# Kernel tuning notes

Measured on AMD Instinct MI355X. Metric: run time of the kernel, lower is better.

Reference implementation:

```python
import jax, jax.numpy as jnp
import numpy as np

# Ternary quant: brevitas 2-bit narrow-range signed int quant with const scale 1.0
# -> q(x) = clamp(round(x), -1, 1), values in {-1, 0, 1}

def ternary(x):
    return jnp.clip(jnp.round(x), -1.0, 1.0)

def batchnorm(x, gamma, beta, eps=1e-5):
    # training-mode BatchNorm1d: batch statistics over dim 0 (biased var)
    mean = jnp.mean(x, axis=0)
    var = jnp.var(x, axis=0)
    return (x - mean) * jax.lax.rsqrt(var + eps) * gamma + beta

def tensornorm(x, w, b, eps=1e-4):
    # BNN-PYNQ TensorNorm: normalize over whole tensor (unbiased var), scalar affine
    mean = jnp.mean(x)
    var = jnp.var(x, ddof=1)
    return (x - mean) / jnp.sqrt(var + eps) * w + b


def setup_inputs() -> dict:
    key = jax.random.key(0)
    ks = jax.random.split(key, 4)
    B = 16384
    x = jax.random.uniform(ks[0], (B, 784), dtype=jnp.float32)          # MNIST-like in [0,1]
    W1 = 2.0 * jax.random.uniform(ks[1], (1024, 784), dtype=jnp.float32) - 1.0  # uniform(-1,1)
    W2 = 2.0 * jax.random.uniform(ks[2], (10, 1024), dtype=jnp.float32) - 1.0
    tnk1, tnk2 = jax.random.split(ks[3])
    return {
        "x": x,
        "W1": W1,
        "gamma1": jnp.ones((1024,), jnp.float32),
        "beta1": jnp.zeros((1024,), jnp.float32),
        "W2": W2,
        "gamma2": jnp.ones((10,), jnp.float32),
        "beta2": jnp.zeros((10,), jnp.float32),
        "tn_w": jax.random.uniform(tnk1, (1,), dtype=jnp.float32),
        "tn_b": jax.random.uniform(tnk2, (1,), dtype=jnp.float32),
    }


def reference(x, W1, gamma1, beta1, W2, gamma2, beta2, tn_w, tn_b):
    h = x.reshape(x.shape[0], -1)
    h = 2.0 * h - 1.0                 # input rescale to [-1,1]
    h = ternary(h)                    # QuantIdentity (2-bit act)
    h = h @ ternary(W1).T             # QuantLinear 784->1024, ternary weights, no bias
    h = batchnorm(h, gamma1, beta1)   # BatchNorm1d(1024)
    h = ternary(h)                    # QuantIdentity
    h = h @ ternary(W2).T             # QuantLinear 1024->10
    h = batchnorm(h, gamma2, beta2)   # BatchNorm1d(10)
    h = ternary(h)                    # QuantIdentity
    return tensornorm(h, tn_w, tn_b)  # TensorNorm
```

## Files before the change

### kernel.cpp

```cpp
#include <hip/hip_runtime.h>
#include <stdint.h>

typedef int i32x4 __attribute__((ext_vector_type(4)));
typedef short s16x8 __attribute__((ext_vector_type(8)));
typedef unsigned long long ull;

#define BB 16384
#define KD 784
#define KP 832
#define N1 1024
#define N2 10
#define NTOT (BB * N2)

#define OFF_AQ 0ULL
#define SZ_AQ (13631488ULL)
#define OFF_W1Q (OFF_AQ + SZ_AQ)
#define SZ_W1Q (851968ULL)
#define OFF_W2Q (OFF_W1Q + SZ_W1Q)
#define SZ_W2Q (16384ULL)
#define OFF_C1 (OFF_W2Q + SZ_W2Q)
#define SZ_C1 (33554432ULL)
#define OFF_STATS (OFF_C1 + SZ_C1)
#define SZ_STATS (16384ULL)
#define OFF_BN1 (OFF_STATS + SZ_STATS)
#define SZ_BN1 (16384ULL)
#define OFF_C2 (OFF_BN1 + SZ_BN1)
#define SZ_C2 (1048576ULL)
#define OFF_T2 (OFF_C2 + SZ_C2)
#define SZ_T2 (163840ULL)

__device__ __forceinline__ void async16(const void* g, void* l) {
  __builtin_amdgcn_global_load_lds((__attribute__((address_space(1))) void*)(void*)(g),
                                   (__attribute__((address_space(3))) void*)(l), 16, 0, 0);
}

__device__ __forceinline__ int8_t ternq(float v) {
  float q = rintf(v);
  return q > 0.5f ? 1 : (q < -0.5f ? -1 : 0);
}

__global__ void k0_quant(const float* __restrict__ x, const float* __restrict__ W1,
                         const float* __restrict__ W2, int8_t* __restrict__ Aq,
                         int8_t* __restrict__ W1q, int8_t* __restrict__ W2q,
                         int* __restrict__ stats) {
  const int TA = BB * KP / 16;
  const int TW = N1 * KP / 16;
  const int T2 = N2 * N1 / 16;
  int tid = blockIdx.x * 256 + threadIdx.x;
  if (tid < 4096) stats[tid] = 0;
  union {
    int4 v;
    int8_t b[16];
  } o;
  o.v = make_int4(0, 0, 0, 0);
  if (tid < TA) {
    int base = tid * 16;
    int r = base / KP, k = base - r * KP;
    if (k < KD) {
      const float4* xp = (const float4*)&x[r * KD + k];
#pragma unroll
      for (int g = 0; g < 4; ++g) {
        float4 f = xp[g];
        o.b[g * 4 + 0] = ternq(2.0f * f.x - 1.0f);
        o.b[g * 4 + 1] = ternq(2.0f * f.y - 1.0f);
        o.b[g * 4 + 2] = ternq(2.0f * f.z - 1.0f);
        o.b[g * 4 + 3] = ternq(2.0f * f.w - 1.0f);
      }
    }
    *(int4*)&Aq[base] = o.v;
  } else if (tid < TA + TW) {
    int base = (tid - TA) * 16;
    int r = base / KP, k = base - r * KP;
    if (k < KD) {
      const float4* wp = (const float4*)&W1[r * KD + k];
#pragma unroll
      for (int g = 0; g < 4; ++g) {
        float4 f = wp[g];
        o.b[g * 4 + 0] = ternq(f.x);
        o.b[g * 4 + 1] = ternq(f.y);
        o.b[g * 4 + 2] = ternq(f.z);
        o.b[g * 4 + 3] = ternq(f.w);
      }
    }
    *(int4*)&W1q[base] = o.v;
  } else if (tid < TA + TW + T2) {
    int base = (tid - TA - TW) * 16;
    const float4* wp = (const float4*)&W2[base];
#pragma unroll
    for (int g = 0; g < 4; ++g) {
      float4 f = wp[g];
      o.b[g * 4 + 0] = ternq(f.x);
      o.b[g * 4 + 1] = ternq(f.y);
      o.b[g * 4 + 2] = ternq(f.z);
      o.b[g * 4 + 3] = ternq(f.w);
    }
    *(int4*)&W2q[base] = o.v;
  }
}

__global__ __launch_bounds__(256, 3) void k1_gemm1(const int8_t* __restrict__ Aq,
                                                   const int8_t* __restrict__ W1q,
                                                   short* __restrict__ C1,
                                                   int* __restrict__ colsum,
                                                   ull* __restrict__ colsq) {
  __shared__ int8_t As[128 * 64];
  __shared__ int8_t Bs[128 * 64];
  __shared__ int cS[128];
  __shared__ int cQ[128];
  const int t = threadIdx.x;
  const int lane = t & 63, wave = t >> 6;
  const int wr = wave >> 1, wc = wave & 1;
  const int rowBase = blockIdx.y * 128, colBase = blockIdx.x * 128;
  if (t < 128) {
    cS[t] = 0;
    cQ[t] = 0;
  }

  i32x4 acc[4][4] = {};

  const int r0 = t >> 2;
  const int gsrc = ((t & 3) ^ ((t >> 3) & 3)) * 16;
  const int m = lane & 15;
  const int goff = ((lane >> 4) ^ ((m >> 1) & 3)) * 16;

  for (int kt = 0; kt < KP / 64; ++kt) {
    __syncthreads();
    const int kb = kt * 64;
    async16(&Aq[(size_t)(rowBase + r0) * KP + kb + gsrc], &As[t * 16]);
    async16(&Aq[(size_t)(rowBase + r0 + 64) * KP + kb + gsrc], &As[4096 + t * 16]);
    async16(&W1q[(size_t)(colBase + r0) * KP + kb + gsrc], &Bs[t * 16]);
    async16(&W1q[(size_t)(colBase + r0 + 64) * KP + kb + gsrc], &Bs[4096 + t * 16]);
    __syncthreads();
    i32x4 av[4], bv[4];
#pragma unroll
    for (int i = 0; i < 4; ++i) av[i] = *(const i32x4*)&As[(64 * wr + 16 * i + m) * 64 + goff];
#pragma unroll
    for (int j = 0; j < 4; ++j) bv[j] = *(const i32x4*)&Bs[(64 * wc + 16 * j + m) * 64 + goff];
#pragma unroll
    for (int i = 0; i < 4; ++i)
#pragma unroll
      for (int j = 0; j < 4; ++j)
        acc[i][j] = __builtin_amdgcn_mfma_i32_16x16x64_i8(av[i], bv[j], acc[i][j], 0, 0, 0);
  }

  const int q = lane >> 4, cl = lane & 15;
#pragma unroll
  for (int j = 0; j < 4; ++j) {
    const int colLoc = 64 * wc + 16 * j + cl;
    const int col = colBase + colLoc;
    int s = 0, sq = 0;
#pragma unroll
    for (int i = 0; i < 4; ++i) {
#pragma unroll
      for (int rg = 0; rg < 4; ++rg) {
        int v = acc[i][j][rg];
        int row = rowBase + 64 * wr + 16 * i + q * 4 + rg;
        C1[(size_t)row * N1 + col] = (short)v;
        s += v;
        sq += v * v;
      }
    }
    atomicAdd(&cS[colLoc], s);
    atomicAdd(&cQ[colLoc], sq);
  }
  __syncthreads();
  if (t < 128) {
    atomicAdd(&colsum[colBase + t], cS[t]);
    atomicAdd(&colsq[colBase + t], (ull)(unsigned)cQ[t]);
  }
}

__global__ void k3_bn1(const int* __restrict__ colsum, const ull* __restrict__ colsq,
                       const float* __restrict__ g1, const float* __restrict__ b1,
                       double* __restrict__ Ac, double* __restrict__ Bc) {
  int c = blockIdx.x * 256 + threadIdx.x;
  double mean = (double)colsum[c] / 16384.0;
  double var = (double)colsq[c] / 16384.0 - mean * mean;
  double dinv = 1.0 / sqrt(var + 1e-5);
  double a = dinv * (double)g1[c];
  Ac[c] = a;
  Bc[c] = (double)b1[c] - mean * a;
}

#define W2S 1040
__global__ __launch_bounds__(256) void k45_bnq_gemm2(
    const short* __restrict__ C1, const double* __restrict__ Ac, const double* __restrict__ Bc,
    const int8_t* __restrict__ W2q, int* __restrict__ C2, int* __restrict__ sum2p,
    ull* __restrict__ sq2p) {
  __shared__ double AcS[N1];
  __shared__ double BcS[N1];
  __shared__ int8_t W2s[16 * W2S];
  __shared__ int cS[16];
  __shared__ int cQ[16];
  const int t = threadIdx.x;
  for (int i = t; i < N1; i += 256) {
    AcS[i] = Ac[i];
    BcS[i] = Bc[i];
  }
  for (int i = t; i < 1024; i += 256) {
    int r = i >> 6, c16 = (i & 63) * 16;
    *(int4*)&W2s[r * W2S + c16] = *(const int4*)&W2q[r * N1 + c16];
  }
  if (t < 16) {
    cS[t] = 0;
    cQ[t] = 0;
  }
  __syncthreads();

  const int lane = t & 63, wave = t >> 6;
  const int m = lane & 15, kc = lane >> 4;
  const int tile = blockIdx.x * 4 + wave;
  const int rowBase = tile * 16;
  const short* arow = &C1[(size_t)(rowBase + m) * N1];

  i32x4 acc = {0, 0, 0, 0};
#pragma unroll
  for (int kt = 0; kt < 16; ++kt) {
    const int k0 = kt * 64 + kc * 16;
    s16x8 v0 = *(const s16x8*)&arow[k0];
    s16x8 v1 = *(const s16x8*)&arow[k0 + 8];
    union {
      i32x4 v;
      int8_t b[16];
    } afr;
#pragma unroll
    for (int j = 0; j < 8; ++j) {
      double z = (double)v0[j] * AcS[k0 + j] + BcS[k0 + j];
      double qq = rint(z);
      qq = qq < -1.0 ? -1.0 : (qq > 1.0 ? 1.0 : qq);
      afr.b[j] = (int8_t)qq;
    }
#pragma unroll
    for (int j = 0; j < 8; ++j) {
      double z = (double)v1[j] * AcS[k0 + 8 + j] + BcS[k0 + 8 + j];
      double qq = rint(z);
      qq = qq < -1.0 ? -1.0 : (qq > 1.0 ? 1.0 : qq);
      afr.b[8 + j] = (int8_t)qq;
    }
    i32x4 bfr = *(const i32x4*)&W2s[m * W2S + k0];
    acc = __builtin_amdgcn_mfma_i32_16x16x64_i8(afr.v, bfr, acc, 0, 0, 0);
  }

  const int col = m;
#pragma unroll
  for (int rg = 0; rg < 4; ++rg) C2[(rowBase + kc * 4 + rg) * 16 + col] = acc[rg];
  if (col < N2) {
    int s = 0, sq = 0;
#pragma unroll
    for (int rg = 0; rg < 4; ++rg) {
      int v = acc[rg];
      s += v;
      sq += v * v;
    }
    atomicAdd(&cS[col], s);
    atomicAdd(&cQ[col], sq);
  }
  __syncthreads();
  if (t < N2) {
    atomicAdd(&sum2p[t * 16], cS[t]);
    atomicAdd(&sq2p[t * 8], (ull)(unsigned)cQ[t]);
  }
}

__global__ __launch_bounds__(256) void k7_bn2q(const int* __restrict__ C2,
                                               const int* __restrict__ sum2p,
                                               const ull* __restrict__ sq2p,
                                               const float* __restrict__ g2,
                                               const float* __restrict__ b2,
                                               int8_t* __restrict__ t2, int* __restrict__ gsum,
                                               int* __restrict__ gsq) {
  int s = 0, sq = 0;
  for (int id = blockIdx.x * 256 + threadIdx.x; id < NTOT; id += gridDim.x * 256) {
    int r = id / N2, c = id - r * N2;
    int v = C2[r * 16 + c];
    double mean = (double)sum2p[c * 16] / 16384.0;
    double var = (double)sq2p[c * 8] / 16384.0 - mean * mean;
    double z = ((double)v - mean) / sqrt(var + 1e-5) * (double)g2[c] + (double)b2[c];
    double qq = rint(z);
    qq = qq < -1.0 ? -1.0 : (qq > 1.0 ? 1.0 : qq);
    int ti = (int)qq;
    t2[id] = (int8_t)ti;
    s += ti;
    sq += ti * ti;
  }
#pragma unroll
  for (int off = 32; off > 0; off >>= 1) {
    s += __shfl_xor(s, off, 64);
    sq += __shfl_xor(sq, off, 64);
  }
  __shared__ int bs, bq;
  if (threadIdx.x == 0) {
    bs = 0;
    bq = 0;
  }
  __syncthreads();
  if ((threadIdx.x & 63) == 0) {
    atomicAdd(&bs, s);
    atomicAdd(&bq, sq);
  }
  __syncthreads();
  if (threadIdx.x == 0) {
    atomicAdd(gsum, bs);
    atomicAdd(gsq, bq);
  }
}

__global__ void k9_out(const int8_t* __restrict__ t2, const int* __restrict__ gsum,
                       const int* __restrict__ gsq, const float* __restrict__ tn_w,
                       const float* __restrict__ tn_b, float* __restrict__ out) {
  int id = blockIdx.x * 256 + threadIdx.x;
  double n = (double)NTOT;
  double sm = (double)*gsum;
  double mean = sm / n;
  double var = ((double)*gsq - sm * sm / n) / (n - 1.0);
  double alpha = (double)tn_w[0] / sqrt(var + 1e-4);
  out[id] = (float)(((double)t2[id] - mean) * alpha + (double)tn_b[0]);
}

extern "C" void kernel_launch(void* const* d_in, const int* in_sizes, int n_in, void* d_out,
                              int out_size, void* d_ws, size_t ws_size, hipStream_t stream) {
  const float* x = (const float*)d_in[0];
  const float* W1 = (const float*)d_in[1];
  const float* g1 = (const float*)d_in[2];
  const float* b1 = (const float*)d_in[3];
  const float* W2 = (const float*)d_in[4];
  const float* g2 = (const float*)d_in[5];
  const float* b2 = (const float*)d_in[6];
  const float* tnw = (const float*)d_in[7];
  const float* tnb = (const float*)d_in[8];

  char* ws = (char*)d_ws;
  int8_t* Aq = (int8_t*)(ws + OFF_AQ);
  int8_t* W1q = (int8_t*)(ws + OFF_W1Q);
  int8_t* W2q = (int8_t*)(ws + OFF_W2Q);
  short* C1 = (short*)(ws + OFF_C1);
  int* statsZ = (int*)(ws + OFF_STATS);
  int* colsum = (int*)(ws + OFF_STATS);
  ull* colsq = (ull*)(ws + OFF_STATS + 4096);
  int* sum2p = (int*)(ws + OFF_STATS + 12288);
  ull* sq2p = (ull*)(ws + OFF_STATS + 13312);
  int* gsum = (int*)(ws + OFF_STATS + 14336);
  int* gsq = (int*)(ws + OFF_STATS + 14400);
  double* Ac = (double*)(ws + OFF_BN1);
  double* Bc = (double*)(ws + OFF_BN1 + 8192);
  int* C2 = (int*)(ws + OFF_C2);
  int8_t* t2 = (int8_t*)(ws + OFF_T2);

  const int totalT = BB * KP / 16 + N1 * KP / 16 + N2 * N1 / 16;
  k0_quant<<<(totalT + 255) / 256, 256, 0, stream>>>(x, W1, W2, Aq, W1q, W2q, statsZ);
  k1_gemm1<<<dim3(8, 128), 256, 0, stream>>>(Aq, W1q, C1, colsum, colsq);
  k3_bn1<<<4, 256, 0, stream>>>(colsum, colsq, g1, b1, Ac, Bc);
  k45_bnq_gemm2<<<256, 256, 0, stream>>>(C1, Ac, Bc, W2q, C2, sum2p, sq2p);
  k7_bn2q<<<160, 256, 0, stream>>>(C2, sum2p, sq2p, g2, b2, t2, gsum, gsq);
  k9_out<<<NTOT / 256, 256, 0, stream>>>(t2, gsum, gsq, tnw, tnb, (float*)d_out);
}
```

Baseline: 157.8 us.

## Widen GEMM1 K-tile to 128 and fold BN1 coefficient kernel into GEMM2

The first GEMM now stages 128-wide K slices (K padded to 896) with an 8-way XOR swizzle and runs two MFMA sub-steps per tile, halving the number of barrier-separated load phases. The separate BN1 coefficient kernel is removed, and each GEMM2 block recomputes the per-column scale and shift from the column sums directly. This saves one launch and a round trip through global memory. In exchange, GEMM1 uses more LDS (which may lower occupancy), does extra padded K work, and the BN1 math is repeated redundantly in every GEMM2 block.

```diff
diff --git a/kernel.cpp b/kernel.cpp
--- a/kernel.cpp
+++ b/kernel.cpp
@@ -7,24 +7,22 @@
 
 #define BB 16384
 #define KD 784
-#define KP 832
+#define KP 896
 #define N1 1024
 #define N2 10
 #define NTOT (BB * N2)
 
 #define OFF_AQ 0ULL
-#define SZ_AQ (13631488ULL)
+#define SZ_AQ (14680064ULL)
 #define OFF_W1Q (OFF_AQ + SZ_AQ)
-#define SZ_W1Q (851968ULL)
+#define SZ_W1Q (917504ULL)
 #define OFF_W2Q (OFF_W1Q + SZ_W1Q)
 #define SZ_W2Q (16384ULL)
 #define OFF_C1 (OFF_W2Q + SZ_W2Q)
 #define SZ_C1 (33554432ULL)
 #define OFF_STATS (OFF_C1 + SZ_C1)
 #define SZ_STATS (16384ULL)
-#define OFF_BN1 (OFF_STATS + SZ_STATS)
-#define SZ_BN1 (16384ULL)
-#define OFF_C2 (OFF_BN1 + SZ_BN1)
+#define OFF_C2 (OFF_STATS + SZ_STATS)
 #define SZ_C2 (1048576ULL)
 #define OFF_T2 (OFF_C2 + SZ_C2)
 #define SZ_T2 (163840ULL)
@@ -103,8 +101,8 @@
                                                    short* __restrict__ C1,
                                                    int* __restrict__ colsum,
                                                    ull* __restrict__ colsq) {
-  __shared__ int8_t As[128 * 64];
-  __shared__ int8_t Bs[128 * 64];
+  __shared__ int8_t As[128 * 128];
+  __shared__ int8_t Bs[128 * 128];
   __shared__ int cS[128];
   __shared__ int cQ[128];
   const int t = threadIdx.x;
@@ -117,30 +115,45 @@
   }
 
   i32x4 acc[4][4] = {};
-
-  const int r0 = t >> 2;
-  const int gsrc = ((t & 3) ^ ((t >> 3) & 3)) * 16;
-  const int m = lane & 15;
-  const int goff = ((lane >> 4) ^ ((m >> 1) & 3)) * 16;
-
-  for (int kt = 0; kt < KP / 64; ++kt) {
+  const int m = lane & 15, kc = lane >> 4;
+
+  int srow[4], sgo[4];
+#pragma unroll
+  for (int s = 0; s < 4; ++s) {
+    int c = t + 256 * s;
+    srow[s] = c >> 3;
+    sgo[s] = ((c & 7) ^ (srow[s] & 7)) * 16;
+  }
+
+  for (int kt = 0; kt < 7; ++kt) {
     __syncthreads();
-    const int kb = kt * 64;
-    async16(&Aq[(size_t)(rowBase + r0) * KP + kb + gsrc], &As[t * 16]);
-    async16(&Aq[(size_t)(rowBase + r0 + 64) * KP + kb + gsrc], &As[4096 + t * 16]);
-    async16(&W1q[(size_t)(colBase + r0) * KP + kb + gsrc], &Bs[t * 16]);
-    async16(&W1q[(size_t)(colBase + r0 + 64) * KP + kb + gsrc], &Bs[4096 + t * 16]);
+    const int kb = kt * 128;
+#pragma unroll
+    for (int s = 0; s < 4; ++s) {
+      int c = t + 256 * s;
+      async16(&Aq[(size_t)(rowBase + srow[s]) * KP + kb + sgo[s]], &As[c * 16]);
+      async16(&W1q[(size_t)(colBase + srow[s]) * KP + kb + sgo[s]], &Bs[c * 16]);
+    }
     __syncthreads();
-    i32x4 av[4], bv[4];
-#pragma unroll
-    for (int i = 0; i < 4; ++i) av[i] = *(const i32x4*)&As[(64 * wr + 16 * i + m) * 64 + goff];
-#pragma unroll
-    for (int j = 0; j < 4; ++j) bv[j] = *(const i32x4*)&Bs[(64 * wc + 16 * j + m) * 64 + goff];
-#pragma unroll
-    for (int i = 0; i < 4; ++i)
-#pragma unroll
-      for (int j = 0; j < 4; ++j)
-        acc[i][j] = __builtin_amdgcn_mfma_i32_16x16x64_i8(av[i], bv[j], acc[i][j], 0, 0, 0);
+#pragma unroll
+    for (int h = 0; h < 2; ++h) {
+      i32x4 av[4], bv[4];
+#pragma unroll
+      for (int i = 0; i < 4; ++i) {
+        int row = 64 * wr + 16 * i + m;
+        av[i] = *(const i32x4*)&As[row * 128 + (((4 * h + kc) ^ (row & 7)) * 16)];
+      }
+#pragma unroll
+      for (int j = 0; j < 4; ++j) {
+        int row = 64 * wc + 16 * j + m;
+        bv[j] = *(const i32x4*)&Bs[row * 128 + (((4 * h + kc) ^ (row & 7)) * 16)];
+      }
+#pragma unroll
+      for (int i = 0; i < 4; ++i)
+#pragma unroll
+        for (int j = 0; j < 4; ++j)
+          acc[i][j] = __builtin_amdgcn_mfma_i32_16x16x64_i8(av[i], bv[j], acc[i][j], 0, 0, 0);
+    }
   }
 
   const int q = lane >> 4, cl = lane & 15;
@@ -170,23 +183,11 @@
   }
 }
 
-__global__ void k3_bn1(const int* __restrict__ colsum, const ull* __restrict__ colsq,
-                       const float* __restrict__ g1, const float* __restrict__ b1,
-                       double* __restrict__ Ac, double* __restrict__ Bc) {
-  int c = blockIdx.x * 256 + threadIdx.x;
-  double mean = (double)colsum[c] / 16384.0;
-  double var = (double)colsq[c] / 16384.0 - mean * mean;
-  double dinv = 1.0 / sqrt(var + 1e-5);
-  double a = dinv * (double)g1[c];
-  Ac[c] = a;
-  Bc[c] = (double)b1[c] - mean * a;
-}
-
 #define W2S 1040
 __global__ __launch_bounds__(256) void k45_bnq_gemm2(
-    const short* __restrict__ C1, const double* __restrict__ Ac, const double* __restrict__ Bc,
-    const int8_t* __restrict__ W2q, int* __restrict__ C2, int* __restrict__ sum2p,
-    ull* __restrict__ sq2p) {
+    const short* __restrict__ C1, const int* __restrict__ colsum, const ull* __restrict__ colsq,
+    const float* __restrict__ g1, const float* __restrict__ b1, const int8_t* __restrict__ W2q,
+    int* __restrict__ C2, int* __restrict__ sum2p, ull* __restrict__ sq2p) {
   __shared__ double AcS[N1];
   __shared__ double BcS[N1];
   __shared__ int8_t W2s[16 * W2S];
@@ -194,8 +195,11 @@
   __shared__ int cQ[16];
   const int t = threadIdx.x;
   for (int i = t; i < N1; i += 256) {
-    AcS[i] = Ac[i];
-    BcS[i] = Bc[i];
+    double mean = (double)colsum[i] / 16384.0;
+    double var = (double)colsq[i] / 16384.0 - mean * mean;
+    double a = (double)g1[i] / sqrt(var + 1e-5);
+    AcS[i] = a;
+    BcS[i] = (double)b1[i] - mean * a;
   }
   for (int i = t; i < 1024; i += 256) {
     int r = i >> 6, c16 = (i & 63) * 16;
@@ -341,16 +345,13 @@
   ull* sq2p = (ull*)(ws + OFF_STATS + 13312);
   int* gsum = (int*)(ws + OFF_STATS + 14336);
   int* gsq = (int*)(ws + OFF_STATS + 14400);
-  double* Ac = (double*)(ws + OFF_BN1);
-  double* Bc = (double*)(ws + OFF_BN1 + 8192);
   int* C2 = (int*)(ws + OFF_C2);
   int8_t* t2 = (int8_t*)(ws + OFF_T2);
 
   const int totalT = BB * KP / 16 + N1 * KP / 16 + N2 * N1 / 16;
   k0_quant<<<(totalT + 255) / 256, 256, 0, stream>>>(x, W1, W2, Aq, W1q, W2q, statsZ);
   k1_gemm1<<<dim3(8, 128), 256, 0, stream>>>(Aq, W1q, C1, colsum, colsq);
-  k3_bn1<<<4, 256, 0, stream>>>(colsum, colsq, g1, b1, Ac, Bc);
-  k45_bnq_gemm2<<<256, 256, 0, stream>>>(C1, Ac, Bc, W2q, C2, sum2p, sq2p);
+  k45_bnq_gemm2<<<256, 256, 0, stream>>>(C1, colsum, colsq, g1, b1, W2q, C2, sum2p, sq2p);
   k7_bn2q<<<160, 256, 0, stream>>>(C2, sum2p, sq2p, g2, b2, t2, gsum, gsq);
   k9_out<<<NTOT / 256, 256, 0, stream>>>(t2, gsum, gsq, tnw, tnb, (float*)d_out);
 }
```

Measured after the change: 153.8 us. -2.6%, faster.
